# Performance work log

Hardware: AMD Instinct MI355X
Metric: run time of the kernel (lower is better)

## Reference

```python
import jax, jax.numpy as jnp
import numpy as np
from jax import lax

BN_EPS = 1e-5


def _bn(t, g, b, m, v):
    # eval-mode BatchNorm2d over channel axis 1
    scale = (g / jnp.sqrt(v + BN_EPS))[None, :, None, None]
    return (t - m[None, :, None, None]) * scale + b[None, :, None, None]


def _conv1x1(t, w):
    # w: (out_c, in_c)
    return jnp.einsum('bchw,oc->bohw', t, w)


def setup_inputs() -> dict:
    key = jax.random.key(0)
    ks = jax.random.split(key, 8)
    B, C_in, H, W = 16, 640, 32, 32
    x = jax.random.normal(ks[0], (B, C_in, H, W), dtype=jnp.float32)

    def bn_params(k, c):
        k1, k2, k3, k4 = jax.random.split(k, 4)
        return (jax.random.normal(k1, (c,), jnp.float32) * 0.1 + 1.0,  # gamma
                jax.random.normal(k2, (c,), jnp.float32) * 0.1,        # beta
                jax.random.normal(k3, (c,), jnp.float32) * 0.1,        # running mean
                jax.random.uniform(k4, (c,), jnp.float32) + 0.5)       # running var

    bn1_g, bn1_b, bn1_m, bn1_v = bn_params(ks[1], 640)
    w_in = jax.random.normal(ks[2], (64, 640), jnp.float32) / np.sqrt(640)
    bnin_g, bnin_b, bnin_m, bnin_v = bn_params(ks[3], 64)
    w_emb = jax.random.normal(ks[4], (640, 1664), jnp.float32) / np.sqrt(1664)
    bne_g, bne_b, bne_m, bne_v = bn_params(ks[5], 640)
    w_out = jax.random.normal(ks[6], (640, 640), jnp.float32) / np.sqrt(640)
    bno_g, bno_b, bno_m, bno_v = bn_params(ks[7], 640)

    return dict(x=x,
                bn1_g=bn1_g, bn1_b=bn1_b, bn1_m=bn1_m, bn1_v=bn1_v,
                w_in=w_in, bnin_g=bnin_g, bnin_b=bnin_b, bnin_m=bnin_m, bnin_v=bnin_v,
                w_emb=w_emb, bne_g=bne_g, bne_b=bne_b, bne_m=bne_m, bne_v=bne_v,
                w_out=w_out, bno_g=bno_g, bno_b=bno_b, bno_m=bno_m, bno_v=bno_v)


def reference(x,
              bn1_g, bn1_b, bn1_m, bn1_v,
              w_in, bnin_g, bnin_b, bnin_m, bnin_v,
              w_emb, bne_g, bne_b, bne_m, bne_v,
              w_out, bno_g, bno_b, bno_m, bno_v):
    KH, KW = 5, 5
    x = jax.nn.relu(_bn(x, bn1_g, bn1_b, bn1_m, bn1_v))
    x = jax.nn.relu(_bn(_conv1x1(x, w_in), bnin_g, bnin_b, bnin_m, bnin_v))
    x0 = jax.nn.relu(x)  # second ReLU in original forward (no-op but faithful)
    # F.normalize(x, dim=1, p=2), eps=1e-12 (PyTorch default)
    norm = jnp.sqrt(jnp.sum(x0 * x0, axis=1, keepdims=True))
    identity = x0 / jnp.maximum(norm, 1e-12)
    b, c, h, w = identity.shape
    # unfold: (b, c*KH*KW, h, w), channel-major ordering matches torch Unfold
    patches = lax.conv_general_dilated_patches(
        identity, (KH, KW), (1, 1), ((2, 2), (2, 2)))
    corr = patches.reshape(b, c, KH * KW, h, w) * identity[:, :, None, :, :]
    corr = corr.reshape(b, c * KH * KW, h, w)
    # featureL2Norm: sqrt(sum(x^2, 1) + 1e-6)
    gs = corr / jnp.sqrt(jnp.sum(corr * corr, axis=1, keepdims=True) + 1e-6)
    feat = jnp.concatenate([identity, gs], axis=1)  # (b, 1664, h, w)
    e = jax.nn.relu(_bn(_conv1x1(feat, w_emb), bne_g, bne_b, bne_m, bne_v))
    out = _bn(_conv1x1(e, w_out), bno_g, bno_b, bno_m, bno_v)
    # dropout in eval mode = identity
    return out
```

## Files before the change

### kernel.cpp

```cpp
#include <hip/hip_runtime.h>
#include <math.h>

#define BN_EPS 1e-5f

using short8  = __attribute__((ext_vector_type(8))) short;
using f32x16  = __attribute__((ext_vector_type(16))) float;


__device__ __forceinline__ float bflo(unsigned u) { return __uint_as_float(u << 16); }
__device__ __forceinline__ float bfhi(unsigned u) { return __uint_as_float(u & 0xffff0000u); }

__device__ __forceinline__ unsigned bf16_rne(float f) {
    unsigned u = __float_as_uint(f);
    return (u + 0x7fffu + ((u >> 16) & 1u)) >> 16;
}
__device__ __forceinline__ unsigned pack_bf16(float lo, float hi) {
    return bf16_rne(lo) | (bf16_rne(hi) << 16);
}
__device__ __forceinline__ unsigned pk_hu(float lo, float hi) {
    unsigned a = __float_as_uint(lo) + 0x8000u;
    unsigned b = __float_as_uint(hi) + 0x8000u;
    return __builtin_amdgcn_perm(b, a, 0x07060302u);
}
__device__ __forceinline__ unsigned pmul_fast(unsigned a, unsigned b) {
    return pk_hu(bflo(a) * bflo(b), bfhi(a) * bfhi(b));
}

__global__ __launch_bounds__(256)
void k_prep(const float* __restrict__ g1, const float* __restrict__ b1,
            const float* __restrict__ m1, const float* __restrict__ v1,
            const float* __restrict__ w_in,
            const float* __restrict__ gi, const float* __restrict__ bi,
            const float* __restrict__ mi, const float* __restrict__ vi,
            const float* __restrict__ ge, const float* __restrict__ be,
            const float* __restrict__ me, const float* __restrict__ ve,
            const float* __restrict__ w_out,
            const float* __restrict__ go, const float* __restrict__ bo,
            const float* __restrict__ mo, const float* __restrict__ vo,
            float* __restrict__ s1, float* __restrict__ b1c,
            float* __restrict__ biasI, float* __restrict__ biasE, float* __restrict__ biasO,
            unsigned* __restrict__ wIt, unsigned* __restrict__ wOt)
{
    int i = blockIdx.x * 256 + threadIdx.x;

    if (i < 640) {
        float s = g1[i] * rsqrtf(v1[i] + BN_EPS);
        s1[i] = s; b1c[i] = b1[i] - m1[i] * s;
    } else if (i < 704) {
        int c = i - 640;
        float s = gi[c] * rsqrtf(vi[c] + BN_EPS);
        biasI[c] = bi[c] - mi[c] * s;
    } else if (i < 1344) {
        int c = i - 704;
        float s = ge[c] * rsqrtf(ve[c] + BN_EPS);
        biasE[c] = be[c] - me[c] * s;
    } else if (i < 1984) {
        int c = i - 1344;
        float s = go[c] * rsqrtf(vo[c] + BN_EPS);
        biasO[c] = bo[c] - mo[c] * s;
    }

    if (i >= 2048 && i < 7168) {
        int u = i - 2048;
        int kc = u >> 8, w = u & 255;
        int mf = w >> 7, kh = (w >> 6) & 1, sl = w & 63;
        int oc = mf * 32 + (sl & 31);
        int k0 = kc * 32 + kh * 16 + (sl >> 5) * 8;
        float sc = gi[oc] * rsqrtf(vi[oc] + BN_EPS);
        unsigned d[4];
#pragma unroll
        for (int q = 0; q < 4; q++)
            d[q] = pack_bf16(w_in[oc * 640 + k0 + 2 * q] * sc,
                             w_in[oc * 640 + k0 + 2 * q + 1] * sc);
        ((uint4*)wIt)[u] = make_uint4(d[0], d[1], d[2], d[3]);
    }

    if (i >= 8192 && i < 59392) {
        int u = i - 8192;
        int ci = u >> 9, w = u & 511;
        int mt = ci / 20, kc = ci - mt * 20;
        int mf = w >> 7, kh = (w >> 6) & 1, sl = w & 63;
        int oc = mt * 128 + mf * 32 + (sl & 31);
        int k0 = kc * 32 + kh * 16 + (sl >> 5) * 8;
        float sc = go[oc] * rsqrtf(vo[oc] + BN_EPS);
        unsigned d[4];
#pragma unroll
        for (int q = 0; q < 4; q++)
            d[q] = pack_bf16(w_out[oc * 640 + k0 + 2 * q] * sc,
                             w_out[oc * 640 + k0 + 2 * q + 1] * sc);
        ((uint4*)wOt)[u] = make_uint4(d[0], d[1], d[2], d[3]);
    }
}

__global__ __launch_bounds__(256)
void k_prepE(const float* __restrict__ w_emb,
             const float* __restrict__ ge, const float* __restrict__ ve,
             unsigned* __restrict__ wEt)
{
    __shared__ float row[1664];
    const int tid = threadIdx.x;
    const int oc = blockIdx.x;

#pragma unroll
    for (int it = 0; it < 2; it++) {
        int u = it * 256 + tid;
        if (u < 416)
            ((float4*)row)[u] = ((const float4*)&w_emb[(size_t)oc * 1664])[u];
    }
    __syncthreads();

    if (tid < 208) {
        int kc = tid >> 2, kh = (tid >> 1) & 1, ksub = tid & 1;
        int k0 = kc * 32 + kh * 16 + ksub * 8;
        float sc = ge[oc] * rsqrtf(ve[oc] + BN_EPS);
        float v[8];
#pragma unroll
        for (int j = 0; j < 8; j++) {
            int kgp = k0 + j;
            int orig;
            if (kgp < 64) orig = kgp;
            else { int t = kgp - 64; orig = 64 + (t & 63) * 25 + (t >> 6); }
            v[j] = row[orig] * sc;
        }
        int mt = oc >> 7, mf = (oc >> 5) & 3;
        int idx = (mt * 52 + kc) * 512 + (mf * 2 + kh) * 64 + ksub * 32 + (oc & 31);
        ((uint4*)wEt)[idx] = make_uint4(pack_bf16(v[0], v[1]), pack_bf16(v[2], v[3]),
                                        pack_bf16(v[4], v[5]), pack_bf16(v[6], v[7]));
    }
}

__global__ __launch_bounds__(512, 1)
void k_identity(const float* __restrict__ x,
                const float* __restrict__ s1, const float* __restrict__ b1c,
                const unsigned* __restrict__ wIt, const float* __restrict__ biasI,
                unsigned* __restrict__ ident)
{
    __shared__ short smem[2][4096];
    __shared__ float Tpart[64 * 65];
    __shared__ float T[64 * 68];
    __shared__ float inv[64];

    const int tid  = threadIdx.x;
    const int half = tid >> 8;
    const int t    = tid & 255;
    const int l = t & 63, wv = t >> 6;
    const int mf = wv >> 1, nf = wv & 1;
    const int p0 = blockIdx.x * 64;
    const int b = p0 >> 10, hw0 = p0 & 1023;

    f32x16 acc;
#pragma unroll
    for (int r = 0; r < 16; r++) acc[r] = 0.f;

    for (int i = 0; i < 10; i++) {
        const int kc = half * 10 + i;
        uint4 av = ((const uint4*)wIt)[kc * 256 + t];
        int bnf = t >> 7, bkh = (t >> 6) & 1, sl = t & 63;
        int px = bnf * 32 + (sl & 31);
        int ch0 = kc * 32 + bkh * 16 + (sl >> 5) * 8;
        float4 sA = *(const float4*)&s1[ch0], sB = *(const float4*)&s1[ch0 + 4];
        float4 bA = *(const float4*)&b1c[ch0], bB = *(const float4*)&b1c[ch0 + 4];
        float vv[8];
        const float* xp = &x[((size_t)b * 640 + ch0) * 1024 + hw0 + px];
        vv[0] = fmaxf(fmaf(xp[0], sA.x, bA.x), 0.f);
        vv[1] = fmaxf(fmaf(xp[1024], sA.y, bA.y), 0.f);
        vv[2] = fmaxf(fmaf(xp[2048], sA.z, bA.z), 0.f);
        vv[3] = fmaxf(fmaf(xp[3072], sA.w, bA.w), 0.f);
        vv[4] = fmaxf(fmaf(xp[4096], sB.x, bB.x), 0.f);
        vv[5] = fmaxf(fmaf(xp[5120], sB.y, bB.y), 0.f);
        vv[6] = fmaxf(fmaf(xp[6144], sB.z, bB.z), 0.f);
        vv[7] = fmaxf(fmaf(xp[7168], sB.w, bB.w), 0.f);
        uint4 bvpk = make_uint4(pack_bf16(vv[0], vv[1]), pack_bf16(vv[2], vv[3]),
                                pack_bf16(vv[4], vv[5]), pack_bf16(vv[6], vv[7]));
        __syncthreads();
        ((uint4*)smem[half])[t] = av;
        ((uint4*)(smem[half] + 2048))[t] = bvpk;
        __syncthreads();
#pragma unroll
        for (int kh = 0; kh < 2; kh++) {
            short8 a  = *(const short8*)&smem[half][((mf * 2 + kh) * 64 + l) * 8];
            short8 bb = *(const short8*)&smem[half][2048 + ((nf * 2 + kh) * 64 + l) * 8];
            acc = __builtin_amdgcn_mfma_f32_32x32x16_bf16(a, bb, acc, 0, 0, 0);
        }
    }
    if (half == 1) {
#pragma unroll
        for (int r = 0; r < 16; r++) {
            int m = mf * 32 + (r & 3) + 8 * (r >> 2) + 4 * (l >> 5);
            int px = nf * 32 + (l & 31);
            Tpart[px * 65 + m] = acc[r];
        }
    }
    __syncthreads();
    if (half == 0) {
#pragma unroll
        for (int r = 0; r < 16; r++) {
            int m = mf * 32 + (r & 3) + 8 * (r >> 2) + 4 * (l >> 5);
            int px = nf * 32 + (l & 31);
            float v = acc[r] + Tpart[px * 65 + m];
            T[px * 68 + m] = fmaxf(v + biasI[m], 0.f);
        }
    }
    __syncthreads();
    if (tid < 64) {
        float sum = 0.f;
#pragma unroll 8
        for (int c = 0; c < 64; c++) { float v = T[tid * 68 + c]; sum = fmaf(v, v, sum); }
        inv[tid] = 1.f / fmaxf(sqrtf(sum), 1e-12f);
    }
    __syncthreads();
    {
        int px = tid >> 3, q = tid & 7;
        float iv = inv[px];
        unsigned d[4];
#pragma unroll
        for (int t2 = 0; t2 < 4; t2++)
            d[t2] = pack_bf16(T[px * 68 + q * 8 + 2 * t2] * iv,
                              T[px * 68 + q * 8 + 2 * t2 + 1] * iv);
        *(uint4*)&ident[(size_t)(p0 + px) * 32 + q * 4] = make_uint4(d[0], d[1], d[2], d[3]);
    }
}

#define FS_SLAB 0
#define FS_CTRS 15552
__global__ __launch_bounds__(512, 1)
void k_feat(const unsigned* __restrict__ ident, unsigned* __restrict__ featC, int ptBase)
{
    __shared__ short smem[20160];
    __shared__ float invDs[64];

    const int tid = threadIdx.x;
    const int pt = ptBase + blockIdx.x;
    const int b = pt >> 4, r0 = (pt & 15) * 2;

#pragma unroll
    for (int it = 0; it < 4; it++) {
        int u = it * 512 + tid;
        if (u < 1728) {
            int spx = u >> 3, q = u & 7;
            int sr = spx / 36, sc = spx - sr * 36;
            int r = r0 + sr - 2, c = sc - 2;
            uint4 v = make_uint4(0u, 0u, 0u, 0u);
            if (r >= 0 && r < 32 && c >= 0 && c < 32)
                v = *(const uint4*)&ident[((size_t)(b * 1024 + r * 32 + c) * 64 + q * 8) / 2];
            *(uint4*)&smem[FS_SLAB + spx * 72 + q * 8] = v;
        }
    }
    __syncthreads();

    {
        int px = tid >> 3, part = tid & 7;
        int rh = px >> 5, rw = px & 31;
        float ctr[8];
        const unsigned* cp = (const unsigned*)&smem[FS_SLAB + ((rh + 2) * 36 + rw + 2) * 72 + part * 8];
#pragma unroll
        for (int d = 0; d < 4; d++) { ctr[2 * d] = bflo(cp[d]); ctr[2 * d + 1] = bfhi(cp[d]); }
        float sum = 0.f;
#pragma unroll
        for (int k = 0; k < 25; k++) {
            const int kh = k / 5, kw = k % 5;
            const unsigned* nb = (const unsigned*)&smem[FS_SLAB + ((rh + kh) * 36 + rw + kw) * 72 + part * 8];
#pragma unroll
            for (int d = 0; d < 4; d++) {
                float q0 = bflo(nb[d]) * ctr[2 * d];
                float q1 = bfhi(nb[d]) * ctr[2 * d + 1];
                sum = fmaf(q0, q0, sum); sum = fmaf(q1, q1, sum);
            }
        }
        sum += __shfl_xor(sum, 1);
        sum += __shfl_xor(sum, 2);
        sum += __shfl_xor(sum, 4);
        if (part == 0) invDs[px] = rsqrtf(sum + 1e-6f);
    }
    __syncthreads();

    {
        int px = tid >> 3, q = tid & 7;
        int spx = ((px >> 5) + 2) * 36 + (px & 31) + 2;
        const unsigned* src = (const unsigned*)&smem[FS_SLAB + spx * 72 + q * 8];
        float iv = invDs[px];
        unsigned d[4];
#pragma unroll
        for (int dd = 0; dd < 4; dd++)
            d[dd] = pk_hu(bflo(src[dd]) * iv, bfhi(src[dd]) * iv);
        *(uint4*)&smem[FS_CTRS + px * 72 + q * 8] = make_uint4(d[0], d[1], d[2], d[3]);
    }
    __syncthreads();

    const int t = tid & 255;
    const int hf = t >> 7, bkh = (t >> 6) & 1, sl = t & 63;
    const int pxl = hf * 32 + (sl & 31);
    const int cl = bkh * 16 + (sl >> 5) * 8;
    const int spxC = (hf + 2) * 36 + (sl & 31) + 2;
    const int kcH = tid >> 8;
    uint4* dst = (uint4*)featC + (size_t)blockIdx.x * 52 * 256 + t;

    for (int it = 0; it < 26; it++) {
        int kc = it * 2 + kcH;
        uint4 f;
        if (kc < 2) {
            f = *(const uint4*)&smem[FS_SLAB + spxC * 72 + kc * 32 + cl];
        } else {
            int idx = kc - 2;
            int ksp = idx >> 1;
            int cb = (idx & 1) * 32 + cl;
            int kho = ksp / 5, kwo = ksp - kho * 5;
            int spx = (hf + kho) * 36 + (sl & 31) + kwo;
            const unsigned* nb = (const unsigned*)&smem[FS_SLAB + spx * 72 + cb];
            const unsigned* ct = (const unsigned*)&smem[FS_CTRS + pxl * 72 + cb];
            f = make_uint4(pmul_fast(nb[0], ct[0]), pmul_fast(nb[1], ct[1]),
                           pmul_fast(nb[2], ct[2]), pmul_fast(nb[3], ct[3]));
        }
        dst[kc * 256] = f;
    }
}

__device__ __forceinline__ void ld_frag(const uint4* __restrict__ A, const uint4* __restrict__ B,
                                        int kc, int mh, int nh, int l,
                                        uint4 av[2][2], uint4 bv[2][2])
{
#pragma unroll
    for (int mi = 0; mi < 2; mi++)
#pragma unroll
        for (int kh = 0; kh < 2; kh++)
            av[mi][kh] = A[(size_t)kc * 512 + ((mh * 2 + mi) * 2 + kh) * 64 + l];
#pragma unroll
    for (int ni = 0; ni < 2; ni++) {
        int bnf = 2 * nh + ni;
#pragma unroll
        for (int kh = 0; kh < 2; kh++)
            bv[ni][kh] = B[((size_t)(bnf >> 1) * 52 + kc) * 256 + ((bnf & 1) << 7) + (kh << 6) + l];
    }
}
__device__ __forceinline__ void do_mfma(uint4 av[2][2], uint4 bv[2][2], f32x16 acc[2][2])
{
#pragma unroll
    for (int kh = 0; kh < 2; kh++) {
        acc[0][0] = __builtin_amdgcn_mfma_f32_32x32x16_bf16(*(short8*)&av[0][kh], *(short8*)&bv[0][kh], acc[0][0], 0, 0, 0);
        acc[0][1] = __builtin_amdgcn_mfma_f32_32x32x16_bf16(*(short8*)&av[0][kh], *(short8*)&bv[1][kh], acc[0][1], 0, 0, 0);
        acc[1][0] = __builtin_amdgcn_mfma_f32_32x32x16_bf16(*(short8*)&av[1][kh], *(short8*)&bv[0][kh], acc[1][0], 0, 0, 0);
        acc[1][1] = __builtin_amdgcn_mfma_f32_32x32x16_bf16(*(short8*)&av[1][kh], *(short8*)&bv[1][kh], acc[1][1], 0, 0, 0);
    }
}

__global__ __launch_bounds__(256, 2)
void k_emb(const unsigned* __restrict__ featC, const unsigned* __restrict__ wEt,
           const float* __restrict__ biasE, unsigned* __restrict__ eG, int ntBase)
{
    __shared__ short Ep[128 * 136];

    const int tid = threadIdx.x;
    const int l = tid & 63, wv = tid >> 6;
    const int mh = wv >> 1, nh = wv & 1;
    const int ntL = blockIdx.x, mt = blockIdx.y;

    f32x16 acc[2][2];
#pragma unroll
    for (int i = 0; i < 2; i++)
#pragma unroll
        for (int j = 0; j < 2; j++)
#pragma unroll
            for (int r = 0; r < 16; r++) acc[i][j][r] = 0.f;

    const uint4* A = (const uint4*)wEt + (size_t)(mt * 52) * 512;
    const uint4* B = (const uint4*)featC + (size_t)ntL * 2 * 52 * 256;

    uint4 a0[2][2], b0[2][2], a1[2][2], b1[2][2];
    ld_frag(A, B, 0, mh, nh, l, a0, b0);
    for (int kc = 0; kc < 52; kc += 2) {
        ld_frag(A, B, kc + 1, mh, nh, l, a1, b1);
        do_mfma(a0, b0, acc);
        if (kc + 2 < 52) ld_frag(A, B, kc + 2, mh, nh, l, a0, b0);
        do_mfma(a1, b1, acc);
    }

#pragma unroll
    for (int mi = 0; mi < 2; mi++)
#pragma unroll
        for (int ni = 0; ni < 2; ni++) {
            int px = (nh * 2 + ni) * 32 + (l & 31);
#pragma unroll
            for (int r = 0; r < 16; r += 2) {
                int m = (mh * 2 + mi) * 32 + (r & 3) + 8 * (r >> 2) + 4 * (l >> 5);
                float v0 = fmaxf(acc[mi][ni][r] + biasE[mt * 128 + m], 0.f);
                float v1 = fmaxf(acc[mi][ni][r + 1] + biasE[mt * 128 + m + 1], 0.f);
                *(unsigned*)&Ep[px * 136 + m] = pack_bf16(v0, v1);
            }
        }
    __syncthreads();
#pragma unroll
    for (int it = 0; it < 8; it++) {
        int w = it * 256 + tid;
        int oct = w >> 7, pxl = w & 127;
        uint4 v = *(const uint4*)&Ep[pxl * 136 + oct * 8];
        int kcp = mt * 4 + (oct >> 2);
        int bkh = (oct >> 1) & 1, ksub = oct & 1;
        int ptg = (ntBase + ntL) * 2 + (pxl >> 6);
        int hf = (pxl >> 5) & 1, sl2 = ksub * 32 + (pxl & 31);
        ((uint4*)eG)[((size_t)ptg * 20 + kcp) * 256 + (hf << 7) + (bkh << 6) + sl2] = v;
    }
}

__device__ __forceinline__ void ld_fragO(const uint4* __restrict__ A, const uint4* __restrict__ B,
                                         int kc, int mh, int nh, int l,
                                         uint4 av[2][2], uint4 bv[2][2])
{
#pragma unroll
    for (int mi = 0; mi < 2; mi++)
#pragma unroll
        for (int kh = 0; kh < 2; kh++)
            av[mi][kh] = A[(size_t)kc * 512 + ((mh * 2 + mi) * 2 + kh) * 64 + l];
#pragma unroll
    for (int ni = 0; ni < 2; ni++) {
        int bnf = 2 * nh + ni;
#pragma unroll
        for (int kh = 0; kh < 2; kh++)
            bv[ni][kh] = B[((size_t)(bnf >> 1) * 20 + kc) * 256 + ((bnf & 1) << 7) + (kh << 6) + l];
    }
}

__global__ __launch_bounds__(256, 2)
void k_out(const unsigned* __restrict__ eG, const unsigned* __restrict__ wOt,
           const float* __restrict__ biasO, float* __restrict__ out)
{
    const int tid = threadIdx.x;
    const int l = tid & 63, wv = tid >> 6;
    const int mh = wv >> 1, nh = wv & 1;
    const int nt = blockIdx.x, mt = blockIdx.y;
    const int p0 = nt * 128;
    const int b = p0 >> 10, hw0 = p0 & 1023;

    f32x16 acc[2][2];
#pragma unroll
    for (int i = 0; i < 2; i++)
#pragma unroll
        for (int j = 0; j < 2; j++)
#pragma unroll
            for (int r = 0; r < 16; r++) acc[i][j][r] = 0.f;

    const uint4* A = (const uint4*)wOt + (size_t)(mt * 20) * 512;
    const uint4* B = (const uint4*)eG + (size_t)nt * 2 * 20 * 256;

    uint4 a0[2][2], b0[2][2], a1[2][2], b1[2][2];
    ld_fragO(A, B, 0, mh, nh, l, a0, b0);
    for (int kc = 0; kc < 20; kc += 2) {
        ld_fragO(A, B, kc + 1, mh, nh, l, a1, b1);
        do_mfma(a0, b0, acc);
        if (kc + 2 < 20) ld_fragO(A, B, kc + 2, mh, nh, l, a0, b0);
        do_mfma(a1, b1, acc);
    }
#pragma unroll
    for (int mi = 0; mi < 2; mi++)
#pragma unroll
        for (int ni = 0; ni < 2; ni++) {
            int pxl = (nh * 2 + ni) * 32 + (l & 31);
#pragma unroll
            for (int r = 0; r < 16; r++) {
                int oc = mt * 128 + (mh * 2 + mi) * 32 + (r & 3) + 8 * (r >> 2) + 4 * (l >> 5);
                out[((size_t)b * 640 + oc) * 1024 + hw0 + pxl] = acc[mi][ni][r] + biasO[oc];
            }
        }
}

extern "C" void kernel_launch(void* const* d_in, const int* in_sizes, int n_in,
                              void* d_out, int out_size, void* d_ws, size_t ws_size,
                              hipStream_t stream)
{
    const float* x    = (const float*)d_in[0];
    const float* g1   = (const float*)d_in[1];
    const float* b1   = (const float*)d_in[2];
    const float* m1   = (const float*)d_in[3];
    const float* v1   = (const float*)d_in[4];
    const float* w_in = (const float*)d_in[5];
    const float* gi   = (const float*)d_in[6];
    const float* bi   = (const float*)d_in[7];
    const float* mi   = (const float*)d_in[8];
    const float* vi   = (const float*)d_in[9];
    const float* w_emb= (const float*)d_in[10];
    const float* ge   = (const float*)d_in[11];
    const float* be   = (const float*)d_in[12];
    const float* me   = (const float*)d_in[13];
    const float* ve   = (const float*)d_in[14];
    const float* w_out= (const float*)d_in[15];
    const float* go   = (const float*)d_in[16];
    const float* bo   = (const float*)d_in[17];
    const float* mo   = (const float*)d_in[18];
    const float* vo   = (const float*)d_in[19];

    char* ws = (char*)d_ws;
    float*    s1    = (float*)(ws + 0);
    float*    b1c   = (float*)(ws + 2560);
    float*    biasI = (float*)(ws + 5120);
    float*    biasE = (float*)(ws + 5376);
    float*    biasO = (float*)(ws + 7936);
    unsigned* wIt   = (unsigned*)(ws + 16384);
    unsigned* wOt   = (unsigned*)(ws + 98304);
    unsigned* wEt   = (unsigned*)(ws + 917504);
    unsigned* ident = (unsigned*)(ws + 3047424);
    unsigned* eG    = (unsigned*)(ws + 5144576);
    float*    out   = (float*)d_out;

    const size_t featFullOff = 26116096ull;
    const size_t featFullBytes = 256ull * 52 * 256 * 16;

    k_prep<<<232, 256, 0, stream>>>(g1, b1, m1, v1, w_in, gi, bi, mi, vi,
                                    ge, be, me, ve, w_out, go, bo, mo, vo,
                                    s1, b1c, biasI, biasE, biasO, wIt, wOt);
    k_prepE<<<640, 256, 0, stream>>>(w_emb, ge, ve, wEt);
    k_identity<<<256, 512, 0, stream>>>(x, s1, b1c, wIt, biasI, ident);

    if (ws_size >= featFullOff + featFullBytes) {
        unsigned* featC = (unsigned*)(ws + featFullOff);
        k_feat<<<256, 512, 0, stream>>>(ident, featC, 0);
        k_emb<<<dim3(128, 5), 256, 0, stream>>>(featC, wEt, biasE, eG, 0);
    } else {
        unsigned* featC = (unsigned*)(ws + 16384);
        for (int c = 0; c < 64; c++) {
            k_feat<<<4, 512, 0, stream>>>(ident, featC, c * 4);
            k_emb<<<dim3(2, 5), 256, 0, stream>>>(featC, wEt, biasE, eG, c * 2);
        }
        k_prep<<<232, 256, 0, stream>>>(g1, b1, m1, v1, w_in, gi, bi, mi, vi,
                                        ge, be, me, ve, w_out, go, bo, mo, vo,
                                        s1, b1c, biasI, biasE, biasO, wIt, wOt);
    }
    k_out<<<dim3(128, 5), 256, 0, stream>>>(eG, wOt, biasO, out);
}
```

Measured before the change: 230.5 us.

## Split emb/out GEMM blocks across 8 waves with smaller per-wave tiles

The k_emb and k_out GEMM kernels now launch 512 threads (8 waves) per block instead of 256. Each wave computes a 64x32 tile with two accumulators instead of a 64x64 tile with four. The explicit double-buffered register prefetch of fragments is dropped in favour of a simple per-k load-then-MFMA loop. The aim is to cut per-wave register pressure and raise the number of resident waves to hide global-load latency. The cost is that A fragments are loaded redundantly by more waves, there is less MFMA work per load, and the software prefetching is gone.

```diff
diff --git a/kernel.cpp b/kernel.cpp
--- a/kernel.cpp
+++ b/kernel.cpp
@@ -315,35 +315,7 @@
     }
 }
 
-__device__ __forceinline__ void ld_frag(const uint4* __restrict__ A, const uint4* __restrict__ B,
-                                        int kc, int mh, int nh, int l,
-                                        uint4 av[2][2], uint4 bv[2][2])
-{
-#pragma unroll
-    for (int mi = 0; mi < 2; mi++)
-#pragma unroll
-        for (int kh = 0; kh < 2; kh++)
-            av[mi][kh] = A[(size_t)kc * 512 + ((mh * 2 + mi) * 2 + kh) * 64 + l];
-#pragma unroll
-    for (int ni = 0; ni < 2; ni++) {
-        int bnf = 2 * nh + ni;
-#pragma unroll
-        for (int kh = 0; kh < 2; kh++)
-            bv[ni][kh] = B[((size_t)(bnf >> 1) * 52 + kc) * 256 + ((bnf & 1) << 7) + (kh << 6) + l];
-    }
-}
-__device__ __forceinline__ void do_mfma(uint4 av[2][2], uint4 bv[2][2], f32x16 acc[2][2])
-{
-#pragma unroll
-    for (int kh = 0; kh < 2; kh++) {
-        acc[0][0] = __builtin_amdgcn_mfma_f32_32x32x16_bf16(*(short8*)&av[0][kh], *(short8*)&bv[0][kh], acc[0][0], 0, 0, 0);
-        acc[0][1] = __builtin_amdgcn_mfma_f32_32x32x16_bf16(*(short8*)&av[0][kh], *(short8*)&bv[1][kh], acc[0][1], 0, 0, 0);
-        acc[1][0] = __builtin_amdgcn_mfma_f32_32x32x16_bf16(*(short8*)&av[1][kh], *(short8*)&bv[0][kh], acc[1][0], 0, 0, 0);
-        acc[1][1] = __builtin_amdgcn_mfma_f32_32x32x16_bf16(*(short8*)&av[1][kh], *(short8*)&bv[1][kh], acc[1][1], 0, 0, 0);
-    }
-}
-
-__global__ __launch_bounds__(256, 2)
+__global__ __launch_bounds__(512, 2)
 void k_emb(const unsigned* __restrict__ featC, const unsigned* __restrict__ wEt,
            const float* __restrict__ biasE, unsigned* __restrict__ eG, int ntBase)
 {
@@ -351,46 +323,50 @@
 
     const int tid = threadIdx.x;
     const int l = tid & 63, wv = tid >> 6;
-    const int mh = wv >> 1, nh = wv & 1;
+    const int mh = wv & 1, nq = wv >> 1;
     const int ntL = blockIdx.x, mt = blockIdx.y;
 
-    f32x16 acc[2][2];
+    f32x16 acc[2];
 #pragma unroll
     for (int i = 0; i < 2; i++)
 #pragma unroll
-        for (int j = 0; j < 2; j++)
-#pragma unroll
-            for (int r = 0; r < 16; r++) acc[i][j][r] = 0.f;
+        for (int r = 0; r < 16; r++) acc[i][r] = 0.f;
 
     const uint4* A = (const uint4*)wEt + (size_t)(mt * 52) * 512;
-    const uint4* B = (const uint4*)featC + (size_t)ntL * 2 * 52 * 256;
-
-    uint4 a0[2][2], b0[2][2], a1[2][2], b1[2][2];
-    ld_frag(A, B, 0, mh, nh, l, a0, b0);
-    for (int kc = 0; kc < 52; kc += 2) {
-        ld_frag(A, B, kc + 1, mh, nh, l, a1, b1);
-        do_mfma(a0, b0, acc);
-        if (kc + 2 < 52) ld_frag(A, B, kc + 2, mh, nh, l, a0, b0);
-        do_mfma(a1, b1, acc);
-    }
-
-#pragma unroll
-    for (int mi = 0; mi < 2; mi++)
-#pragma unroll
-        for (int ni = 0; ni < 2; ni++) {
-            int px = (nh * 2 + ni) * 32 + (l & 31);
-#pragma unroll
-            for (int r = 0; r < 16; r += 2) {
-                int m = (mh * 2 + mi) * 32 + (r & 3) + 8 * (r >> 2) + 4 * (l >> 5);
-                float v0 = fmaxf(acc[mi][ni][r] + biasE[mt * 128 + m], 0.f);
-                float v1 = fmaxf(acc[mi][ni][r + 1] + biasE[mt * 128 + m + 1], 0.f);
-                *(unsigned*)&Ep[px * 136 + m] = pack_bf16(v0, v1);
-            }
-        }
-    __syncthreads();
-#pragma unroll
-    for (int it = 0; it < 8; it++) {
-        int w = it * 256 + tid;
+    const uint4* B = (const uint4*)featC + ((size_t)ntL * 2 + (nq >> 1)) * 52 * 256 + ((nq & 1) << 7) + l;
+
+    for (int kc = 0; kc < 52; kc++) {
+        uint4 av[2][2], bv[2];
+#pragma unroll
+        for (int mi = 0; mi < 2; mi++)
+#pragma unroll
+            for (int kh = 0; kh < 2; kh++)
+                av[mi][kh] = A[(size_t)kc * 512 + (((mh * 2 + mi) * 2 + kh) << 6) + l];
+#pragma unroll
+        for (int kh = 0; kh < 2; kh++)
+            bv[kh] = B[(size_t)kc * 256 + (kh << 6)];
+#pragma unroll
+        for (int kh = 0; kh < 2; kh++) {
+            acc[0] = __builtin_amdgcn_mfma_f32_32x32x16_bf16(*(short8*)&av[0][kh], *(short8*)&bv[kh], acc[0], 0, 0, 0);
+            acc[1] = __builtin_amdgcn_mfma_f32_32x32x16_bf16(*(short8*)&av[1][kh], *(short8*)&bv[kh], acc[1], 0, 0, 0);
+        }
+    }
+
+#pragma unroll
+    for (int mi = 0; mi < 2; mi++) {
+        int px = nq * 32 + (l & 31);
+#pragma unroll
+        for (int r = 0; r < 16; r += 2) {
+            int m = (mh * 2 + mi) * 32 + (r & 3) + 8 * (r >> 2) + 4 * (l >> 5);
+            float v0 = fmaxf(acc[mi][r] + biasE[mt * 128 + m], 0.f);
+            float v1 = fmaxf(acc[mi][r + 1] + biasE[mt * 128 + m + 1], 0.f);
+            *(unsigned*)&Ep[px * 136 + m] = pack_bf16(v0, v1);
+        }
+    }
+    __syncthreads();
+#pragma unroll
+    for (int it = 0; it < 4; it++) {
+        int w = it * 512 + tid;
         int oct = w >> 7, pxl = w & 127;
         uint4 v = *(const uint4*)&Ep[pxl * 136 + oct * 8];
         int kcp = mt * 4 + (oct >> 2);
@@ -401,65 +377,51 @@
     }
 }
 
-__device__ __forceinline__ void ld_fragO(const uint4* __restrict__ A, const uint4* __restrict__ B,
-                                         int kc, int mh, int nh, int l,
-                                         uint4 av[2][2], uint4 bv[2][2])
-{
-#pragma unroll
-    for (int mi = 0; mi < 2; mi++)
-#pragma unroll
-        for (int kh = 0; kh < 2; kh++)
-            av[mi][kh] = A[(size_t)kc * 512 + ((mh * 2 + mi) * 2 + kh) * 64 + l];
-#pragma unroll
-    for (int ni = 0; ni < 2; ni++) {
-        int bnf = 2 * nh + ni;
-#pragma unroll
-        for (int kh = 0; kh < 2; kh++)
-            bv[ni][kh] = B[((size_t)(bnf >> 1) * 20 + kc) * 256 + ((bnf & 1) << 7) + (kh << 6) + l];
-    }
-}
-
-__global__ __launch_bounds__(256, 2)
+__global__ __launch_bounds__(512, 2)
 void k_out(const unsigned* __restrict__ eG, const unsigned* __restrict__ wOt,
            const float* __restrict__ biasO, float* __restrict__ out)
 {
     const int tid = threadIdx.x;
     const int l = tid & 63, wv = tid >> 6;
-    const int mh = wv >> 1, nh = wv & 1;
+    const int mh = wv & 1, nq = wv >> 1;
     const int nt = blockIdx.x, mt = blockIdx.y;
     const int p0 = nt * 128;
     const int b = p0 >> 10, hw0 = p0 & 1023;
 
-    f32x16 acc[2][2];
+    f32x16 acc[2];
 #pragma unroll
     for (int i = 0; i < 2; i++)
 #pragma unroll
-        for (int j = 0; j < 2; j++)
-#pragma unroll
-            for (int r = 0; r < 16; r++) acc[i][j][r] = 0.f;
+        for (int r = 0; r < 16; r++) acc[i][r] = 0.f;
 
     const uint4* A = (const uint4*)wOt + (size_t)(mt * 20) * 512;
-    const uint4* B = (const uint4*)eG + (size_t)nt * 2 * 20 * 256;
-
-    uint4 a0[2][2], b0[2][2], a1[2][2], b1[2][2];
-    ld_fragO(A, B, 0, mh, nh, l, a0, b0);
-    for (int kc = 0; kc < 20; kc += 2) {
-        ld_fragO(A, B, kc + 1, mh, nh, l, a1, b1);
-        do_mfma(a0, b0, acc);
-        if (kc + 2 < 20) ld_fragO(A, B, kc + 2, mh, nh, l, a0, b0);
-        do_mfma(a1, b1, acc);
-    }
-#pragma unroll
-    for (int mi = 0; mi < 2; mi++)
-#pragma unroll
-        for (int ni = 0; ni < 2; ni++) {
-            int pxl = (nh * 2 + ni) * 32 + (l & 31);
-#pragma unroll
-            for (int r = 0; r < 16; r++) {
-                int oc = mt * 128 + (mh * 2 + mi) * 32 + (r & 3) + 8 * (r >> 2) + 4 * (l >> 5);
-                out[((size_t)b * 640 + oc) * 1024 + hw0 + pxl] = acc[mi][ni][r] + biasO[oc];
-            }
-        }
+    const uint4* B = (const uint4*)eG + ((size_t)nt * 2 + (nq >> 1)) * 20 * 256 + ((nq & 1) << 7) + l;
+
+    for (int kc = 0; kc < 20; kc++) {
+        uint4 av[2][2], bv[2];
+#pragma unroll
+        for (int mi = 0; mi < 2; mi++)
+#pragma unroll
+            for (int kh = 0; kh < 2; kh++)
+                av[mi][kh] = A[(size_t)kc * 512 + (((mh * 2 + mi) * 2 + kh) << 6) + l];
+#pragma unroll
+        for (int kh = 0; kh < 2; kh++)
+            bv[kh] = B[(size_t)kc * 256 + (kh << 6)];
+#pragma unroll
+        for (int kh = 0; kh < 2; kh++) {
+            acc[0] = __builtin_amdgcn_mfma_f32_32x32x16_bf16(*(short8*)&av[0][kh], *(short8*)&bv[kh], acc[0], 0, 0, 0);
+            acc[1] = __builtin_amdgcn_mfma_f32_32x32x16_bf16(*(short8*)&av[1][kh], *(short8*)&bv[kh], acc[1], 0, 0, 0);
+        }
+    }
+#pragma unroll
+    for (int mi = 0; mi < 2; mi++) {
+        int pxl = nq * 32 + (l & 31);
+#pragma unroll
+        for (int r = 0; r < 16; r++) {
+            int oc = mt * 128 + (mh * 2 + mi) * 32 + (r & 3) + 8 * (r >> 2) + 4 * (l >> 5);
+            out[((size_t)b * 640 + oc) * 1024 + hw0 + pxl] = acc[mi][r] + biasO[oc];
+        }
+    }
 }
 
 extern "C" void kernel_launch(void* const* d_in, const int* in_sizes, int n_in,
@@ -512,16 +474,16 @@
     if (ws_size >= featFullOff + featFullBytes) {
         unsigned* featC = (unsigned*)(ws + featFullOff);
         k_feat<<<256, 512, 0, stream>>>(ident, featC, 0);
-        k_emb<<<dim3(128, 5), 256, 0, stream>>>(featC, wEt, biasE, eG, 0);
+        k_emb<<<dim3(128, 5), 512, 0, stream>>>(featC, wEt, biasE, eG, 0);
     } else {
         unsigned* featC = (unsigned*)(ws + 16384);
         for (int c = 0; c < 64; c++) {
             k_feat<<<4, 512, 0, stream>>>(ident, featC, c * 4);
-            k_emb<<<dim3(2, 5), 256, 0, stream>>>(featC, wEt, biasE, eG, c * 2);
+            k_emb<<<dim3(2, 5), 512, 0, stream>>>(featC, wEt, biasE, eG, c * 2);
         }
         k_prep<<<232, 256, 0, stream>>>(g1, b1, m1, v1, w_in, gi, bi, mi, vi,
                                         ge, be, me, ve, w_out, go, bo, mo, vo,
                                         s1, b1c, biasI, biasE, biasO, wIt, wOt);
     }
-    k_out<<<dim3(128, 5), 256, 0, stream>>>(eG, wOt, biasO, out);
-}
+    k_out<<<dim3(128, 5), 512, 0, stream>>>(eG, wOt, biasO, out);
+}
```

Result: slower. 246.1 us (+6.7%).
